# Kernel tuning notes

Hardware: AMD Instinct MI355X
Metric: run time of the kernel (lower is better)

Reference implementation:

```python
import jax, jax.numpy as jnp
import numpy as np

LN_EPS = 1e-5


def setup_inputs() -> dict:
    key = jax.random.key(0)
    ks = jax.random.split(key, 10)
    b, n, m, d, e = 2, 4096, 32, 128, 64
    return {
        "t_ij": jax.random.normal(ks[0], (b, n, m, d), dtype=jnp.float32),
        "x1": jax.random.normal(ks[1], (b, n, d, 3), dtype=jnp.float32),
        "x2": jax.random.normal(ks[2], (b, n, d, 5), dtype=jnp.float32),
        "neighbor_indices": jax.random.randint(ks[3], (b, n, m), 0, n),
        "to_queries": jax.random.normal(ks[4], (d, e), dtype=jnp.float32),
        "to_keys1": jax.random.normal(ks[5], (d, e), dtype=jnp.float32),
        "to_keys2": jax.random.normal(ks[6], (d, e), dtype=jnp.float32),
        "ln_weight": jnp.ones((2 * e,), dtype=jnp.float32),
        "edge_w": jax.random.normal(ks[7], (2 * e, d), dtype=jnp.float32) / np.sqrt(2 * e),
        "res_w": jax.random.normal(ks[8], (d, d), dtype=jnp.float32) / np.sqrt(d),
    }


def _degree_inner_product(xl, to_queries, to_keys, neighbor_indices):
    # xl: [b n d ml]; projections over channel dim d -> e
    q = jnp.einsum('bndm,de->bnem', xl, to_queries)   # [b n e ml]
    k = jnp.einsum('bndm,de->bnem', xl, to_keys)      # [b n e ml]
    # gather neighbor keys: [b n j e ml]
    kg = jax.vmap(lambda kk, idx: kk[idx])(k, neighbor_indices)
    # inner product over multiplicity ml, per feature e: [b n j e]
    return jnp.einsum('bnem,bnjem->bnje', q, kg)


def reference(t_ij, x1, x2, neighbor_indices, to_queries, to_keys1, to_keys2,
              ln_weight, edge_w, res_w):
    ip1 = _degree_inner_product(x1, to_queries, to_keys1, neighbor_indices)
    ip2 = _degree_inner_product(x2, to_queries, to_keys2, neighbor_indices)
    w_ij = jnp.concatenate([ip1, ip2], axis=-1)  # [b n j 2e]
    # LayerNorm over last dim, weight only (bias=False)
    mu = jnp.mean(w_ij, axis=-1, keepdims=True)
    var = jnp.mean((w_ij - mu) ** 2, axis=-1, keepdims=True)
    w_ij = (w_ij - mu) * jax.lax.rsqrt(var + LN_EPS) * ln_weight
    edge_out = jax.nn.sigmoid(jnp.einsum('bnje,ed->bnjd', w_ij, edge_w))
    res_out = jnp.einsum('bnjd,de->bnje', t_ij, res_w)
    return edge_out + res_out
```

## Files before the change

### kernel.cpp

```cpp
#include <hip/hip_runtime.h>

#define B_ 2
#define N_ 4096
#define M_ 32
#define D_ 128
#define E_ 64
#define LN_EPS 1e-5f
#define WST 136
#define TOT (B_ * N_)
#define FGRID 768

typedef __bf16 bf16x8 __attribute__((ext_vector_type(8)));
typedef float  f32x4  __attribute__((ext_vector_type(4)));

__global__ __launch_bounds__(256) void proj_kernel(
    const float* __restrict__ x1, const float* __restrict__ x2,
    const float* __restrict__ Wq, const float* __restrict__ Wk1,
    const float* __restrict__ Wk2,
    float* __restrict__ qws, __bf16* __restrict__ kws)
{
    __shared__ float xs[4][D_ * 8];
    const int lane = threadIdx.x & 63;
    const int wv   = threadIdx.x >> 6;
    const int bn   = blockIdx.x * 4 + wv;
    float* xw = xs[wv];
    const float* __restrict__ x1p = x1 + (size_t)bn * (D_ * 3);
    const float* __restrict__ x2p = x2 + (size_t)bn * (D_ * 5);
    for (int i = lane; i < D_ * 3; i += 64) xw[(i / 3) * 8 + (i % 3)]     = x1p[i];
    for (int i = lane; i < D_ * 5; i += 64) xw[(i / 5) * 8 + 3 + (i % 5)] = x2p[i];
    __syncthreads();

    float q[8] = {0.f,0.f,0.f,0.f,0.f,0.f,0.f,0.f};
    float k[8] = {0.f,0.f,0.f,0.f,0.f,0.f,0.f,0.f};
    #pragma unroll 4
    for (int d = 0; d < D_; ++d) {
        const float4 xa = *(const float4*)&xw[d * 8];
        const float4 xb = *(const float4*)&xw[d * 8 + 4];
        const float wq  = Wq [d * E_ + lane];
        const float wk1 = Wk1[d * E_ + lane];
        const float wk2 = Wk2[d * E_ + lane];
        q[0] += xa.x * wq;  q[1] += xa.y * wq;  q[2] += xa.z * wq;  q[3] += xa.w * wq;
        q[4] += xb.x * wq;  q[5] += xb.y * wq;  q[6] += xb.z * wq;  q[7] += xb.w * wq;
        k[0] += xa.x * wk1; k[1] += xa.y * wk1; k[2] += xa.z * wk1;
        k[3] += xa.w * wk2; k[4] += xb.x * wk2; k[5] += xb.y * wk2;
        k[6] += xb.z * wk2; k[7] += xb.w * wk2;
    }
    float4* qo = (float4*)(qws + ((size_t)bn * E_ + lane) * 8);
    qo[0] = make_float4(q[0], q[1], q[2], q[3]);
    qo[1] = make_float4(q[4], q[5], q[6], q[7]);
    bf16x8 kb;
    #pragma unroll
    for (int s = 0; s < 8; ++s) kb[s] = (__bf16)k[s];
    *(bf16x8*)(kws + ((size_t)bn * E_ + lane) * 8) = kb;
}

__device__ __forceinline__ float dpp_red16(float v) {
    v += __int_as_float(__builtin_amdgcn_update_dpp(0, __float_as_int(v), 0xB1,  0xF, 0xF, true));
    v += __int_as_float(__builtin_amdgcn_update_dpp(0, __float_as_int(v), 0x4E,  0xF, 0xF, true));
    v += __int_as_float(__builtin_amdgcn_update_dpp(0, __float_as_int(v), 0x141, 0xF, 0xF, true));
    v += __int_as_float(__builtin_amdgcn_update_dpp(0, __float_as_int(v), 0x140, 0xF, 0xF, true));
    return v;
}
__device__ __forceinline__ float wave_sum(float v) {
    v = dpp_red16(v);
    v += __int_as_float(__builtin_amdgcn_ds_swizzle(__float_as_int(v), 0x401F));
    v += __shfl_xor(v, 32, 64);
    return v;
}

__global__ __launch_bounds__(256, 3) void fused_kernel(
    const float* __restrict__ t_ij, const int* __restrict__ nidx,
    const float* __restrict__ qws, const __bf16* __restrict__ kws,
    const float* __restrict__ ln_w,
    const float* __restrict__ edge_w, const float* __restrict__ res_w,
    float* __restrict__ out)
{
    __shared__ __bf16 wbuf[3][M_ * WST];

    const int t    = threadIdx.x;
    const int lane = t & 63;
    const int wvu  = t >> 6;
    const int r16  = lane & 15;
    const int quad = lane >> 4;
    const int n0   = wvu * 32;

    bf16x8 bE[2][4], bR[2][4];
    #pragma unroll
    for (int nt = 0; nt < 2; ++nt) {
        const int col = n0 + nt * 16 + r16;
        #pragma unroll
        for (int ks = 0; ks < 4; ++ks) {
            const int k0 = ks * 32 + quad * 8;
            bf16x8 fe, fr;
            #pragma unroll
            for (int j = 0; j < 8; ++j) {
                fe[j] = (__bf16)edge_w[(k0 + j) * D_ + col];
                fr[j] = (__bf16)res_w [(k0 + j) * D_ + col];
            }
            bE[nt][ks] = fe;
            bR[nt][ks] = fr;
        }
    }

    const float lnlo = ln_w[lane];
    const float lnhi = ln_w[64 + lane];

    auto phaseW = [&](int bn, __bf16* buf) {
        const int    b  = bn >> 12;
        const size_t jb = (size_t)bn * M_;
        const float* qp = qws + ((size_t)bn * E_ + lane) * 8;
        const float4 qa = *(const float4*)qp;
        const float4 qb = *(const float4*)(qp + 4);
        #pragma unroll 4
        for (int jj = 0; jj < 8; ++jj) {
            const int j  = wvu * 8 + jj;
            const int nj = nidx[jb + j];
            const bf16x8 kv =
                *(const bf16x8*)&kws[((size_t)(b * N_ + nj) * E_ + lane) * 8];
            const float wlo = qa.x * (float)kv[0] + qa.y * (float)kv[1]
                            + qa.z * (float)kv[2];
            const float whi = qa.w * (float)kv[3] + qb.x * (float)kv[4]
                            + qb.y * (float)kv[5] + qb.z * (float)kv[6]
                            + qb.w * (float)kv[7];
            const float s1 = wave_sum(wlo + whi);
            const float s2 = wave_sum(wlo * wlo + whi * whi);
            const float mu  = s1 * (1.f / 128.f);
            const float var = fmaxf(s2 * (1.f / 128.f) - mu * mu, 0.f);
            const float rs  = rsqrtf(var + LN_EPS);
            buf[j * WST + lane]      = (__bf16)((wlo - mu) * rs * lnlo);
            buf[j * WST + 64 + lane] = (__bf16)((whi - mu) * rs * lnhi);
        }
    };

    auto tload = [&](int bn, bf16x8* tf) {
        const float* tp = t_ij + ((size_t)bn * M_ + r16) * D_;
        #pragma unroll
        for (int ks = 0; ks < 4; ++ks) {
            const int ko = ks * 32 + quad * 8;
            const float4 t0 = *(const float4*)(tp + ko);
            const float4 t1 = *(const float4*)(tp + ko + 4);
            bf16x8 a;
            a[0]=(__bf16)t0.x; a[1]=(__bf16)t0.y; a[2]=(__bf16)t0.z; a[3]=(__bf16)t0.w;
            a[4]=(__bf16)t1.x; a[5]=(__bf16)t1.y; a[6]=(__bf16)t1.z; a[7]=(__bf16)t1.w;
            tf[ks] = a;
        }
    };

    auto phaseM = [&](int bn, const __bf16* buf, const bf16x8* tf) {
        const size_t jb = (size_t)bn * M_;
        bf16x8 aT1[4];
        {
            const float* tp = t_ij + (jb + 16 + r16) * D_;
            #pragma unroll
            for (int ks = 0; ks < 4; ++ks) {
                const int ko = ks * 32 + quad * 8;
                const float4 t0 = *(const float4*)(tp + ko);
                const float4 t1 = *(const float4*)(tp + ko + 4);
                bf16x8 a;
                a[0]=(__bf16)t0.x; a[1]=(__bf16)t0.y; a[2]=(__bf16)t0.z; a[3]=(__bf16)t0.w;
                a[4]=(__bf16)t1.x; a[5]=(__bf16)t1.y; a[6]=(__bf16)t1.z; a[7]=(__bf16)t1.w;
                aT1[ks] = a;
            }
        }
        f32x4 accE[2][2], accR[2][2];
        #pragma unroll
        for (int mt = 0; mt < 2; ++mt)
            #pragma unroll
            for (int nt = 0; nt < 2; ++nt) {
                accE[mt][nt] = (f32x4){0.f,0.f,0.f,0.f};
                accR[mt][nt] = (f32x4){0.f,0.f,0.f,0.f};
            }
        #pragma unroll
        for (int ks = 0; ks < 4; ++ks) {
            const bf16x8 aW0 = *(const bf16x8*)&buf[r16 * WST + ks * 32 + quad * 8];
            const bf16x8 aW1 = *(const bf16x8*)&buf[(16 + r16) * WST + ks * 32 + quad * 8];
            #pragma unroll
            for (int nt = 0; nt < 2; ++nt) {
                accE[0][nt] = __builtin_amdgcn_mfma_f32_16x16x32_bf16(bE[nt][ks], aW0,     accE[0][nt], 0, 0, 0);
                accR[0][nt] = __builtin_amdgcn_mfma_f32_16x16x32_bf16(bR[nt][ks], tf[ks],  accR[0][nt], 0, 0, 0);
                accE[1][nt] = __builtin_amdgcn_mfma_f32_16x16x32_bf16(bE[nt][ks], aW1,     accE[1][nt], 0, 0, 0);
                accR[1][nt] = __builtin_amdgcn_mfma_f32_16x16x32_bf16(bR[nt][ks], aT1[ks], accR[1][nt], 0, 0, 0);
            }
        }
        #pragma unroll
        for (int mt = 0; mt < 2; ++mt)
            #pragma unroll
            for (int nt = 0; nt < 2; ++nt) {
                float4 o;
                #pragma unroll
                for (int rr = 0; rr < 4; ++rr) {
                    const float e  = accE[mt][nt][rr];
                    const float sg = __builtin_amdgcn_rcpf(1.f + __expf(-e));
                    (&o.x)[rr] = sg + accR[mt][nt][rr];
                }
                *(float4*)(out + (jb + mt * 16 + r16) * D_ + n0 + nt * 16 + quad * 4) = o;
            }
    };

    const int stride = gridDim.x;
    int bn = blockIdx.x;
    bf16x8 tf[4];
    phaseW(bn, wbuf[0]);
    tload(bn, tf);
    int buf = 0;
    for (; bn < TOT; bn += stride) {
        const int nb   = bn + stride;
        const int nbuf = (buf == 2) ? 0 : buf + 1;
        if (nb < TOT) phaseW(nb, wbuf[nbuf]);
        __syncthreads();
        phaseM(bn, wbuf[buf], tf);
        if (nb < TOT) tload(nb, tf);
        buf = nbuf;
    }
}

extern "C" void kernel_launch(void* const* d_in, const int* in_sizes, int n_in,
                              void* d_out, int out_size, void* d_ws, size_t ws_size,
                              hipStream_t stream) {
    const float* t_ij = (const float*)d_in[0];
    const float* x1   = (const float*)d_in[1];
    const float* x2   = (const float*)d_in[2];
    const int*   nidx = (const int*)  d_in[3];
    const float* Wq   = (const float*)d_in[4];
    const float* Wk1  = (const float*)d_in[5];
    const float* Wk2  = (const float*)d_in[6];
    const float* lnw  = (const float*)d_in[7];
    const float* eww  = (const float*)d_in[8];
    const float* rww  = (const float*)d_in[9];
    float* out = (float*)d_out;

    float*  qws = (float*)d_ws;
    __bf16* kws = (__bf16*)(qws + (size_t)TOT * E_ * 8);

    proj_kernel<<<TOT / 4, 256, 0, stream>>>(x1, x2, Wq, Wk1, Wk2, qws, kws);
    fused_kernel<<<FGRID, 256, 0, stream>>>(t_ij, nidx, qws, kws, lnw, eww, rww, out);
}
```

Before: 370.3 us.

## Stage t_ij tile through LDS with coalesced nontemporal loads and interleaved W layout

Each wave now loads the t_ij tile with contiguous 64-byte-per-lane nontemporal loads and writes it to a triple-buffered LDS tile. Before, each lane gathered strided fragments directly in MFMA layout, and the second half was loaded synchronously inside the matmul phase. The normalized W row is written as interleaved bf16 pairs, and the edge_w rows are permuted to match, so each lane does one 4-byte LDS store. Output stores become nontemporal and the phaseW loop is fully unrolled. LDS use doubles, which may lower occupancy (3 blocks per CU, about 52 KB each), and there are extra LDS reads per matmul step.

```diff
diff --git a/kernel.cpp b/kernel.cpp
--- a/kernel.cpp
+++ b/kernel.cpp
@@ -11,6 +11,7 @@
 #define FGRID 768
 
 typedef __bf16 bf16x8 __attribute__((ext_vector_type(8)));
+typedef __bf16 bf16x2 __attribute__((ext_vector_type(2)));
 typedef float  f32x4  __attribute__((ext_vector_type(4)));
 
 __global__ __launch_bounds__(256) void proj_kernel(
@@ -75,7 +76,7 @@
     const float* __restrict__ edge_w, const float* __restrict__ res_w,
     float* __restrict__ out)
 {
-    __shared__ __bf16 wbuf[3][M_ * WST];
+    __shared__ __bf16 sbuf[3][2][M_ * WST];
 
     const int t    = threadIdx.x;
     const int lane = t & 63;
@@ -94,8 +95,10 @@
             bf16x8 fe, fr;
             #pragma unroll
             for (int j = 0; j < 8; ++j) {
-                fe[j] = (__bf16)edge_w[(k0 + j) * D_ + col];
-                fr[j] = (__bf16)res_w [(k0 + j) * D_ + col];
+                const int kk = k0 + j;
+                const int f  = (kk & 1) ? 64 + (kk >> 1) : (kk >> 1);
+                fe[j] = (__bf16)edge_w[f * D_ + col];
+                fr[j] = (__bf16)res_w [kk * D_ + col];
             }
             bE[nt][ks] = fe;
             bR[nt][ks] = fr;
@@ -105,13 +108,13 @@
     const float lnlo = ln_w[lane];
     const float lnhi = ln_w[64 + lane];
 
-    auto phaseW = [&](int bn, __bf16* buf) {
+    auto phaseW = [&](int bn, __bf16* wb) {
         const int    b  = bn >> 12;
         const size_t jb = (size_t)bn * M_;
         const float* qp = qws + ((size_t)bn * E_ + lane) * 8;
         const float4 qa = *(const float4*)qp;
         const float4 qb = *(const float4*)(qp + 4);
-        #pragma unroll 4
+        #pragma unroll
         for (int jj = 0; jj < 8; ++jj) {
             const int j  = wvu * 8 + jj;
             const int nj = nidx[jb + j];
@@ -127,41 +130,35 @@
             const float mu  = s1 * (1.f / 128.f);
             const float var = fmaxf(s2 * (1.f / 128.f) - mu * mu, 0.f);
             const float rs  = rsqrtf(var + LN_EPS);
-            buf[j * WST + lane]      = (__bf16)((wlo - mu) * rs * lnlo);
-            buf[j * WST + 64 + lane] = (__bf16)((whi - mu) * rs * lnhi);
+            bf16x2 p;
+            p[0] = (__bf16)((wlo - mu) * rs * lnlo);
+            p[1] = (__bf16)((whi - mu) * rs * lnhi);
+            *(bf16x2*)&wb[j * WST + 2 * lane] = p;
         }
     };
 
-    auto tload = [&](int bn, bf16x8* tf) {
-        const float* tp = t_ij + ((size_t)bn * M_ + r16) * D_;
-        #pragma unroll
-        for (int ks = 0; ks < 4; ++ks) {
-            const int ko = ks * 32 + quad * 8;
-            const float4 t0 = *(const float4*)(tp + ko);
-            const float4 t1 = *(const float4*)(tp + ko + 4);
-            bf16x8 a;
-            a[0]=(__bf16)t0.x; a[1]=(__bf16)t0.y; a[2]=(__bf16)t0.z; a[3]=(__bf16)t0.w;
-            a[4]=(__bf16)t1.x; a[5]=(__bf16)t1.y; a[6]=(__bf16)t1.z; a[7]=(__bf16)t1.w;
-            tf[ks] = a;
-        }
+    auto stageT = [&](int bn, __bf16* tb) {
+        const int row = wvu * 8 + (lane >> 3);
+        const int c0  = (lane & 7) * 16;
+        const float* tp = t_ij + ((size_t)bn * M_ + row) * D_ + c0;
+        const f32x4 t0 = __builtin_nontemporal_load((const f32x4*)tp);
+        const f32x4 t1 = __builtin_nontemporal_load((const f32x4*)(tp + 4));
+        const f32x4 t2 = __builtin_nontemporal_load((const f32x4*)(tp + 8));
+        const f32x4 t3 = __builtin_nontemporal_load((const f32x4*)(tp + 12));
+        bf16x8 a0, a1;
+        #pragma unroll
+        for (int r = 0; r < 4; ++r) {
+            a0[r]     = (__bf16)t0[r];
+            a0[4 + r] = (__bf16)t1[r];
+            a1[r]     = (__bf16)t2[r];
+            a1[4 + r] = (__bf16)t3[r];
+        }
+        *(bf16x8*)&tb[row * WST + c0]     = a0;
+        *(bf16x8*)&tb[row * WST + c0 + 8] = a1;
     };
 
-    auto phaseM = [&](int bn, const __bf16* buf, const bf16x8* tf) {
+    auto phaseM = [&](int bn, const __bf16* wb, const __bf16* tb) {
         const size_t jb = (size_t)bn * M_;
-        bf16x8 aT1[4];
-        {
-            const float* tp = t_ij + (jb + 16 + r16) * D_;
-            #pragma unroll
-            for (int ks = 0; ks < 4; ++ks) {
-                const int ko = ks * 32 + quad * 8;
-                const float4 t0 = *(const float4*)(tp + ko);
-                const float4 t1 = *(const float4*)(tp + ko + 4);
-                bf16x8 a;
-                a[0]=(__bf16)t0.x; a[1]=(__bf16)t0.y; a[2]=(__bf16)t0.z; a[3]=(__bf16)t0.w;
-                a[4]=(__bf16)t1.x; a[5]=(__bf16)t1.y; a[6]=(__bf16)t1.z; a[7]=(__bf16)t1.w;
-                aT1[ks] = a;
-            }
-        }
         f32x4 accE[2][2], accR[2][2];
         #pragma unroll
         for (int mt = 0; mt < 2; ++mt)
@@ -172,44 +169,49 @@
             }
         #pragma unroll
         for (int ks = 0; ks < 4; ++ks) {
-            const bf16x8 aW0 = *(const bf16x8*)&buf[r16 * WST + ks * 32 + quad * 8];
-            const bf16x8 aW1 = *(const bf16x8*)&buf[(16 + r16) * WST + ks * 32 + quad * 8];
+            const int off = ks * 32 + quad * 8;
+            const bf16x8 aW0 = *(const bf16x8*)&wb[r16 * WST + off];
+            const bf16x8 aW1 = *(const bf16x8*)&wb[(16 + r16) * WST + off];
+            const bf16x8 tW0 = *(const bf16x8*)&tb[r16 * WST + off];
+            const bf16x8 tW1 = *(const bf16x8*)&tb[(16 + r16) * WST + off];
             #pragma unroll
             for (int nt = 0; nt < 2; ++nt) {
-                accE[0][nt] = __builtin_amdgcn_mfma_f32_16x16x32_bf16(bE[nt][ks], aW0,     accE[0][nt], 0, 0, 0);
-                accR[0][nt] = __builtin_amdgcn_mfma_f32_16x16x32_bf16(bR[nt][ks], tf[ks],  accR[0][nt], 0, 0, 0);
-                accE[1][nt] = __builtin_amdgcn_mfma_f32_16x16x32_bf16(bE[nt][ks], aW1,     accE[1][nt], 0, 0, 0);
-                accR[1][nt] = __builtin_amdgcn_mfma_f32_16x16x32_bf16(bR[nt][ks], aT1[ks], accR[1][nt], 0, 0, 0);
+                accE[0][nt] = __builtin_amdgcn_mfma_f32_16x16x32_bf16(bE[nt][ks], aW0, accE[0][nt], 0, 0, 0);
+                accR[0][nt] = __builtin_amdgcn_mfma_f32_16x16x32_bf16(bR[nt][ks], tW0, accR[0][nt], 0, 0, 0);
+                accE[1][nt] = __builtin_amdgcn_mfma_f32_16x16x32_bf16(bE[nt][ks], aW1, accE[1][nt], 0, 0, 0);
+                accR[1][nt] = __builtin_amdgcn_mfma_f32_16x16x32_bf16(bR[nt][ks], tW1, accR[1][nt], 0, 0, 0);
             }
         }
         #pragma unroll
         for (int mt = 0; mt < 2; ++mt)
             #pragma unroll
             for (int nt = 0; nt < 2; ++nt) {
-                float4 o;
+                f32x4 o;
                 #pragma unroll
                 for (int rr = 0; rr < 4; ++rr) {
                     const float e  = accE[mt][nt][rr];
                     const float sg = __builtin_amdgcn_rcpf(1.f + __expf(-e));
-                    (&o.x)[rr] = sg + accR[mt][nt][rr];
+                    o[rr] = sg + accR[mt][nt][rr];
                 }
-                *(float4*)(out + (jb + mt * 16 + r16) * D_ + n0 + nt * 16 + quad * 4) = o;
+                __builtin_nontemporal_store(o,
+                    (f32x4*)(out + (jb + mt * 16 + r16) * D_ + n0 + nt * 16 + quad * 4));
             }
     };
 
     const int stride = gridDim.x;
     int bn = blockIdx.x;
-    bf16x8 tf[4];
-    phaseW(bn, wbuf[0]);
-    tload(bn, tf);
+    phaseW(bn, sbuf[0][0]);
+    stageT(bn, sbuf[0][1]);
     int buf = 0;
     for (; bn < TOT; bn += stride) {
         const int nb   = bn + stride;
         const int nbuf = (buf == 2) ? 0 : buf + 1;
-        if (nb < TOT) phaseW(nb, wbuf[nbuf]);
+        if (nb < TOT) {
+            phaseW(nb, sbuf[nbuf][0]);
+            stageT(nb, sbuf[nbuf][1]);
+        }
         __syncthreads();
-        phaseM(bn, wbuf[buf], tf);
-        if (nb < TOT) tload(nb, tf);
+        phaseM(bn, sbuf[buf][0], sbuf[buf][1]);
         buf = nbuf;
     }
 }
```

New measurement: 348.7 us. 1.06x faster.
